# Kernel optimization log

Hardware: AMD Instinct MI355X
Metric: run time of the kernel (lower is better)

Reference implementation:

```python
import jax, jax.numpy as jnp
import numpy as np

N = 100000
E = 3200000
F_IN = 128
H1, C1 = 2, 16          # conv1: heads=2, out_channels=16, concat -> 32
H2, C2 = 1, 40          # conv2: heads=1, out_channels=num_classes=40
NEG_SLOPE = 0.2


def setup_inputs() -> dict:
    key = jax.random.key(0)
    ks = jax.random.split(key, 12)
    features = jax.random.normal(ks[0], (N, F_IN), dtype=jnp.float32)
    edges = jax.random.randint(ks[1], (2, E), 0, N, dtype=jnp.int64)
    weight = jax.random.uniform(ks[2], (E,), dtype=jnp.float32)  # ignored (edge_dim=None)
    s = 0.1
    W1 = jax.random.normal(ks[3], (F_IN, H1 * C1), dtype=jnp.float32) * s
    att_src1 = jax.random.normal(ks[4], (H1, C1), dtype=jnp.float32) * s
    att_dst1 = jax.random.normal(ks[5], (H1, C1), dtype=jnp.float32) * s
    b1 = jnp.zeros((H1 * C1,), dtype=jnp.float32)
    W2 = jax.random.normal(ks[6], (H1 * C1, H2 * C2), dtype=jnp.float32) * s
    att_src2 = jax.random.normal(ks[7], (H2, C2), dtype=jnp.float32) * s
    att_dst2 = jax.random.normal(ks[8], (H2, C2), dtype=jnp.float32) * s
    b2 = jnp.zeros((H2 * C2,), dtype=jnp.float32)
    return {"features": features, "edges": edges, "weight": weight,
            "W1": W1, "att_src1": att_src1, "att_dst1": att_dst1, "b1": b1,
            "W2": W2, "att_src2": att_src2, "att_dst2": att_dst2, "b2": b2}


def _segment_softmax(e, seg, num_segments):
    # e: [E, H]; softmax over edges sharing the same destination node
    m = jax.ops.segment_max(e, seg, num_segments=num_segments)
    ex = jnp.exp(e - m[seg])
    s = jax.ops.segment_sum(ex, seg, num_segments=num_segments)
    return ex / (s[seg] + 1e-16)


def _gat_conv(x, src, dst, W, att_src, att_dst, bias, heads, out_ch):
    n = x.shape[0]
    h = (x @ W).reshape(n, heads, out_ch)                  # [N,H,C]
    a_src = jnp.sum(h * att_src, axis=-1)                  # [N,H]
    a_dst = jnp.sum(h * att_dst, axis=-1)                  # [N,H]
    e = a_src[src] + a_dst[dst]                            # [E,H]
    e = jnp.where(e > 0, e, NEG_SLOPE * e)                 # LeakyReLU(0.2)
    alpha = _segment_softmax(e, dst, n)                    # [E,H]
    msg = h[src] * alpha[:, :, None]                       # [E,H,C]
    out = jax.ops.segment_sum(msg, dst, num_segments=n)    # [N,H,C]
    return out.reshape(n, heads * out_ch) + bias           # concat=True


def reference(features, edges, weight, W1, att_src1, att_dst1, b1,
              W2, att_src2, att_dst2, b2):
    n = features.shape[0]
    # GATConv default add_self_loops=True (self-loop removal of pre-existing
    # loops skipped: negligible for random edges and not jit-shape-friendly)
    loop = jnp.arange(n, dtype=edges.dtype)
    src = jnp.concatenate([edges[0], loop])
    dst = jnp.concatenate([edges[1], loop])
    x = _gat_conv(features, src, dst, W1, att_src1, att_dst1, b1, H1, C1)
    x = jax.nn.relu(x)
    # F.dropout with training=self.training -> identity in eval mode
    x = _gat_conv(x, src, dst, W2, att_src2, att_dst2, b2, H2, C2)
    return x
```

## Files before the change

kernel.cpp:

```cpp
#include <hip/hip_runtime.h>


#define DEVFN __device__ __forceinline__
#define CB_SHIFT 8
#define CB_SZ 256
#define CHUNK 2048
#define HIST_MAX 512
#define A2B 240

DEVFN unsigned short f2h(float f) {
  _Float16 h = (_Float16)f;
  unsigned short u;
  __builtin_memcpy(&u, &h, 2);
  return u;
}
DEVFN float h2f(unsigned short u) {
  _Float16 h;
  __builtin_memcpy(&h, &u, 2);
  return (float)h;
}

DEVFN float lrelu(float e) { return e > 0.f ? e : 0.2f * e; }

DEVFN void acc8(float* acc, float x, uint4 u) {
  acc[0] = fmaf(x, h2f(u.x & 0xffff), acc[0]);
  acc[1] = fmaf(x, h2f(u.x >> 16),    acc[1]);
  acc[2] = fmaf(x, h2f(u.y & 0xffff), acc[2]);
  acc[3] = fmaf(x, h2f(u.y >> 16),    acc[3]);
  acc[4] = fmaf(x, h2f(u.z & 0xffff), acc[4]);
  acc[5] = fmaf(x, h2f(u.z >> 16),    acc[5]);
  acc[6] = fmaf(x, h2f(u.w & 0xffff), acc[6]);
  acc[7] = fmaf(x, h2f(u.w >> 16),    acc[7]);
}

DEVFN void read_edge(const long long* eg64, const int* eg32, int is64, int E,
                     int i, int& s, int& d) {
  if (i >= E) { s = d = i - E; return; }
  if (is64) { s = (int)eg64[i]; d = (int)eg64[E + i]; }
  else      { s = eg32[i];      d = eg32[E + i]; }
}

DEVFN int detect64(const int* eg32, int E, int i0, int t) {
  int base = i0;
  if (base > E - 64) base = E - 64;
  if (base < 0) base = 0;
  int i = base + (t & 63);
  unsigned long long m = __ballot((i < E) && (eg32[2 * i + 1] != 0));
  return m == 0ull;
}

__global__ void scan_blocks(const int* __restrict__ cnt, int* __restrict__ rp,
                            int* __restrict__ bsum, int n) {
  __shared__ int buf[2][1024];
  int t = threadIdx.x;
  int gid = blockIdx.x * 1024 + t;
  int v = (gid < n) ? cnt[gid] : 0;
  buf[0][t] = v;
  __syncthreads();
  int pin = 0;
  for (int offd = 1; offd < 1024; offd <<= 1) {
    int nv = buf[pin][t];
    if (t >= offd) nv += buf[pin][t - offd];
    buf[1 - pin][t] = nv;
    pin = 1 - pin;
    __syncthreads();
  }
  int inc = buf[pin][t];
  if (gid < n) rp[gid] = inc - v;
  if (t == 1023) bsum[blockIdx.x] = inc;
}

__global__ void scan_sums(const int* __restrict__ bsum, int* __restrict__ boff,
                          int nb) {
  __shared__ int buf[2][1024];
  __shared__ int carry;
  int t = threadIdx.x;
  if (t == 0) carry = 0;
  __syncthreads();
  for (int base = 0; base < nb; base += 1024) {
    int v = (base + t < nb) ? bsum[base + t] : 0;
    buf[0][t] = v;
    __syncthreads();
    int pin = 0;
    for (int off = 1; off < 1024; off <<= 1) {
      int nv = buf[pin][t];
      if (t >= off) nv += buf[pin][t - off];
      buf[1 - pin][t] = nv;
      pin = 1 - pin;
      __syncthreads();
    }
    if (base + t < nb) boff[base + t] = carry + buf[pin][t] - v;
    __syncthreads();
    if (t == 0) carry += buf[pin][1023];
    __syncthreads();
  }
}

__global__ void scan_add(int* rp, const int* boff, int n, int total) {
  int i = blockIdx.x * 1024 + threadIdx.x;
  if (i < n) rp[i] = rp[i] + boff[blockIdx.x];
  if (i == 0) rp[n] = total;
}

__global__ __launch_bounds__(256) void chunk_hist(const long long* eg64,
                                                  const int* eg32,
                                                  int E, int N, int NWG,
                                                  int* __restrict__ histg) {
  __shared__ int lh[HIST_MAX];
  int w = blockIdx.x, t = threadIdx.x;
  int NB2 = (N + CB_SZ - 1) / CB_SZ;
  for (int j = t; j < NB2; j += 256) lh[j] = 0;
  int i0 = w * CHUNK;
  int is64 = detect64(eg32, E, i0, t);
  __syncthreads();
  int EN = E + N;
  int i1 = i0 + CHUNK; if (i1 > EN) i1 = EN;
  for (int i = i0 + t; i < i1; i += 256) {
    int d;
    if (i >= E) d = i - E;
    else d = is64 ? (int)eg64[E + i] : eg32[E + i];
    atomicAdd(&lh[d >> CB_SHIFT], 1);
  }
  __syncthreads();
  for (int b = t; b < NB2; b += 256) histg[b * NWG + w] = lh[b];
}

__global__ __launch_bounds__(256) void chunk_scatter(const long long* eg64,
                                                     const int* eg32,
                                                     int E, int N, int NWG,
                                                     const int* __restrict__ hists,
                                                     int* __restrict__ tmp) {
  __shared__ int lcur[HIST_MAX];
  int w = blockIdx.x, t = threadIdx.x;
  int NB2 = (N + CB_SZ - 1) / CB_SZ;
  for (int b = t; b < NB2; b += 256) lcur[b] = hists[b * NWG + w];
  int i0 = w * CHUNK;
  int is64 = detect64(eg32, E, i0, t);
  __syncthreads();
  int EN = E + N;
  int i1 = i0 + CHUNK; if (i1 > EN) i1 = EN;
  for (int i = i0 + t; i < i1; i += 256) {
    int s, d;
    read_edge(eg64, eg32, is64, E, i, s, d);
    int b = d >> CB_SHIFT;
    int pos = atomicAdd(&lcur[b], 1);
    tmp[pos] = (s << CB_SHIFT) | (d & (CB_SZ - 1));
  }
}

__global__ __launch_bounds__(256) void bucket_rp_sort(const int* __restrict__ hists,
                                                      int NWG,
                                                      const int* __restrict__ tmp,
                                                      int* __restrict__ rp,
                                                      int* __restrict__ csr,
                                                      int N, int EN) {
  __shared__ int lc[CB_SZ];
  __shared__ int ps[256];
  __shared__ int lcur[CB_SZ];
  int b = blockIdx.x, t = threadIdx.x;
  lc[t] = 0;
  __syncthreads();
  int w0 = hists[b * NWG];
  int w1 = hists[(b + 1) * NWG];
  for (int p = w0 + t; p < w1; p += 256)
    atomicAdd(&lc[tmp[p] & (CB_SZ - 1)], 1);
  __syncthreads();
  int a = lc[t];
  ps[t] = a;
  __syncthreads();
  for (int off = 1; off < 256; off <<= 1) {
    int v = ps[t];
    int u = (t >= off) ? ps[t - off] : 0;
    __syncthreads();
    ps[t] = v + u;
    __syncthreads();
  }
  int base = w0 + ps[t] - a;
  lcur[t] = base;
  int n0 = b * CB_SZ;
  if (n0 + t < N) rp[n0 + t] = base;
  if (b == (int)gridDim.x - 1 && t == 0) rp[N] = EN;
  __syncthreads();
  for (int p = w0 + t; p < w1; p += 256) {
    int e = tmp[p];
    int pos = atomicAdd(&lcur[e & (CB_SZ - 1)], 1);
    csr[pos] = e >> CB_SHIFT;
  }
}

__global__ __launch_bounds__(256) void gemm1f(const float* __restrict__ X,
                                              const float* __restrict__ W,
                                              const float* __restrict__ att_s,
                                              const float* __restrict__ att_d,
                                              uint4* __restrict__ h1h,
                                              float* __restrict__ as1,
                                              float* __restrict__ ad1, int N) {
  __shared__ float Wl[128 * 32];
  __shared__ float Asl[32], Adl[32];
  int t = threadIdx.x;
  for (int i = t; i < 1024; i += 256)
    ((float4*)Wl)[i] = ((const float4*)W)[i];
  if (t < 32) { Asl[t] = att_s[t]; Adl[t] = att_d[t]; }
  __syncthreads();
  int n = blockIdx.x * 256 + t;
  if (n >= N) return;
  const float4* X4 = (const float4*)(X + (size_t)n * 128);
  float acc[32];
#pragma unroll
  for (int c = 0; c < 32; c++) acc[c] = 0.f;
  for (int k4 = 0; k4 < 32; k4++) {
    float4 x = X4[k4];
    const float4* w4 = (const float4*)(Wl + k4 * 128);
#pragma unroll
    for (int c4 = 0; c4 < 8; c4++) {
      float4 w0 = w4[c4], w1 = w4[8 + c4], w2 = w4[16 + c4], w3 = w4[24 + c4];
      float* A = acc + c4 * 4;
      A[0] = fmaf(x.x, w0.x, A[0]); A[1] = fmaf(x.x, w0.y, A[1]);
      A[2] = fmaf(x.x, w0.z, A[2]); A[3] = fmaf(x.x, w0.w, A[3]);
      A[0] = fmaf(x.y, w1.x, A[0]); A[1] = fmaf(x.y, w1.y, A[1]);
      A[2] = fmaf(x.y, w1.z, A[2]); A[3] = fmaf(x.y, w1.w, A[3]);
      A[0] = fmaf(x.z, w2.x, A[0]); A[1] = fmaf(x.z, w2.y, A[1]);
      A[2] = fmaf(x.z, w2.z, A[2]); A[3] = fmaf(x.z, w2.w, A[3]);
      A[0] = fmaf(x.w, w3.x, A[0]); A[1] = fmaf(x.w, w3.y, A[1]);
      A[2] = fmaf(x.w, w3.z, A[2]); A[3] = fmaf(x.w, w3.w, A[3]);
    }
  }
  float s0 = 0.f, d0 = 0.f, s1 = 0.f, d1 = 0.f;
#pragma unroll
  for (int c = 0; c < 16; c++) {
    s0 = fmaf(acc[c], Asl[c], s0);
    d0 = fmaf(acc[c], Adl[c], d0);
    s1 = fmaf(acc[16 + c], Asl[16 + c], s1);
    d1 = fmaf(acc[16 + c], Adl[16 + c], d1);
  }
  as1[n * 2] = s0; as1[n * 2 + 1] = s1;
  ad1[n * 2] = d0; ad1[n * 2 + 1] = d1;
#pragma unroll
  for (int j = 0; j < 4; j++) {
    uint4 u;
    u.x = (unsigned)f2h(acc[j * 8 + 0]) | ((unsigned)f2h(acc[j * 8 + 1]) << 16);
    u.y = (unsigned)f2h(acc[j * 8 + 2]) | ((unsigned)f2h(acc[j * 8 + 3]) << 16);
    u.z = (unsigned)f2h(acc[j * 8 + 4]) | ((unsigned)f2h(acc[j * 8 + 5]) << 16);
    u.w = (unsigned)f2h(acc[j * 8 + 6]) | ((unsigned)f2h(acc[j * 8 + 7]) << 16);
    h1h[(size_t)n * 4 + j] = u;
  }
}

__global__ __launch_bounds__(256, 8) void agg1_gemm2(
    const int* __restrict__ rp, const int* __restrict__ csr,
    const float* __restrict__ as, const float* __restrict__ ad,
    const uint4* __restrict__ h1h, const float* __restrict__ b1,
    const float* __restrict__ W2, const float* __restrict__ as2w,
    const float* __restrict__ ad2w, uint4* __restrict__ h2h,
    float* __restrict__ as2, float* __restrict__ ad2, int N) {
  __shared__ float Wl[32 * 40];
  __shared__ float As2l[40], Ad2l[40];
  __shared__ float x1t[16][33];
  __shared__ float h2r[16][41];
  int t = threadIdx.x;
  for (int i = t; i < 320; i += 256)
    ((float4*)Wl)[i] = ((const float4*)W2)[i];
  if (t < 40) { As2l[t] = as2w[t]; Ad2l[t] = ad2w[t]; }
  int nl = t >> 4, r = t & 15;
  int half = r >> 2, cq = r & 3;
  int h = cq >> 1;
  int n = blockIdx.x * 16 + nl;
  float acc[8] = {0, 0, 0, 0, 0, 0, 0, 0};
  float ssum = 0.f;
  if (n < N) {
    int p0 = rp[n], p1 = rp[n + 1];
    float adv = ad[n * 2 + h];
    int p = p0 + half;
    for (; p + 12 < p1; p += 16) {
      int sA = csr[p], sB = csr[p + 4], sC = csr[p + 8], sD = csr[p + 12];
      float eA = as[sA * 2 + h] + adv;
      float eB = as[sB * 2 + h] + adv;
      float eC = as[sC * 2 + h] + adv;
      float eD = as[sD * 2 + h] + adv;
      uint4 uA = h1h[(size_t)sA * 4 + cq];
      uint4 uB = h1h[(size_t)sB * 4 + cq];
      uint4 uC = h1h[(size_t)sC * 4 + cq];
      uint4 uD = h1h[(size_t)sD * 4 + cq];
      float xA = __expf(lrelu(eA));
      float xB = __expf(lrelu(eB));
      float xC = __expf(lrelu(eC));
      float xD = __expf(lrelu(eD));
      ssum += (xA + xB) + (xC + xD);
      acc8(acc, xA, uA);
      acc8(acc, xB, uB);
      acc8(acc, xC, uC);
      acc8(acc, xD, uD);
    }
    if (p < p1) {
      bool vB = p + 4 < p1, vC = p + 8 < p1;
      int pB = vB ? p + 4 : p;
      int pC = vC ? p + 8 : p;
      int sA = csr[p], sB = csr[pB], sC = csr[pC];
      float eA = as[sA * 2 + h] + adv;
      float eB = as[sB * 2 + h] + adv;
      float eC = as[sC * 2 + h] + adv;
      uint4 uA = h1h[(size_t)sA * 4 + cq];
      uint4 uB = h1h[(size_t)sB * 4 + cq];
      uint4 uC = h1h[(size_t)sC * 4 + cq];
      float xA = __expf(lrelu(eA));
      float xB = vB ? __expf(lrelu(eB)) : 0.f;
      float xC = vC ? __expf(lrelu(eC)) : 0.f;
      ssum += xA + xB + xC;
      acc8(acc, xA, uA);
      acc8(acc, xB, uB);
      acc8(acc, xC, uC);
    }
  }
#pragma unroll
  for (int j = 0; j < 8; j++) acc[j] += __shfl_xor(acc[j], 4);
  ssum += __shfl_xor(ssum, 4);
#pragma unroll
  for (int j = 0; j < 8; j++) acc[j] += __shfl_xor(acc[j], 8);
  ssum += __shfl_xor(ssum, 8);
  if (n < N && half == 0) {
    float inv = 1.0f / (ssum + 1e-16f);
    float4 ba = ((const float4*)b1)[cq * 2];
    float4 bb = ((const float4*)b1)[cq * 2 + 1];
    int ch0 = cq * 8;
    x1t[nl][ch0 + 0] = fmaxf(fmaf(acc[0], inv, ba.x), 0.f);
    x1t[nl][ch0 + 1] = fmaxf(fmaf(acc[1], inv, ba.y), 0.f);
    x1t[nl][ch0 + 2] = fmaxf(fmaf(acc[2], inv, ba.z), 0.f);
    x1t[nl][ch0 + 3] = fmaxf(fmaf(acc[3], inv, ba.w), 0.f);
    x1t[nl][ch0 + 4] = fmaxf(fmaf(acc[4], inv, bb.x), 0.f);
    x1t[nl][ch0 + 5] = fmaxf(fmaf(acc[5], inv, bb.y), 0.f);
    x1t[nl][ch0 + 6] = fmaxf(fmaf(acc[6], inv, bb.z), 0.f);
    x1t[nl][ch0 + 7] = fmaxf(fmaf(acc[7], inv, bb.w), 0.f);
  }
  __syncthreads();
  if (n < N && r < 8) {
    float acc2[5] = {0, 0, 0, 0, 0};
    int cb = r * 5;
    for (int k = 0; k < 32; k++) {
      float x = x1t[nl][k];
#pragma unroll
      for (int c = 0; c < 5; c++)
        acc2[c] = fmaf(x, Wl[k * 40 + cb + c], acc2[c]);
    }
    float ss = 0.f, sd = 0.f;
#pragma unroll
    for (int c = 0; c < 5; c++) {
      ss = fmaf(acc2[c], As2l[cb + c], ss);
      sd = fmaf(acc2[c], Ad2l[cb + c], sd);
    }
#pragma unroll
    for (int off = 1; off < 8; off <<= 1) {
      ss += __shfl_xor(ss, off);
      sd += __shfl_xor(sd, off);
    }
    if (r == 0) { as2[n] = ss; ad2[n] = sd; }
#pragma unroll
    for (int c = 0; c < 5; c++) h2r[nl][cb + c] = acc2[c];
  }
  __syncthreads();
  if (n < N && r < 5) {
    const float* hr = h2r[nl] + r * 8;
    uint4 u;
    u.x = (unsigned)f2h(hr[0]) | ((unsigned)f2h(hr[1]) << 16);
    u.y = (unsigned)f2h(hr[2]) | ((unsigned)f2h(hr[3]) << 16);
    u.z = (unsigned)f2h(hr[4]) | ((unsigned)f2h(hr[5]) << 16);
    u.w = (unsigned)f2h(hr[6]) | ((unsigned)f2h(hr[7]) << 16);
    h2h[(size_t)n * 8 + r] = u;
  }
}

__global__ __launch_bounds__(256, 8) void agg2_fused(const int* __restrict__ rp,
                                                     const int* __restrict__ csr,
                                                     const float* __restrict__ as,
                                                     const float* __restrict__ ad,
                                                     const uint4* __restrict__ h2h,
                                                     const float* __restrict__ bias,
                                                     float* __restrict__ outp, int N) {
  __shared__ float part[256][9];
  int t = threadIdx.x;
  int idx = blockIdx.x * A2B + t;
  bool act = (t < A2B) && (idx < N * 20);
  int n = 0, half = 0, cq = 0, p0 = 0, p1 = 0;
  float adv = 0.f;
  if (act) {
    n = idx / 20;
    int rr = idx % 20;
    half = rr / 5;
    cq = rr - half * 5;
    p0 = rp[n]; p1 = rp[n + 1];
    adv = ad[n];
  }
  float acc[8] = {0, 0, 0, 0, 0, 0, 0, 0};
  float ssum = 0.f;
  if (act) {
    int p = p0 + half;
    for (; p + 12 < p1; p += 16) {
      int sA = csr[p], sB = csr[p + 4], sC = csr[p + 8], sD = csr[p + 12];
      float eA = as[sA] + adv;
      float eB = as[sB] + adv;
      float eC = as[sC] + adv;
      float eD = as[sD] + adv;
      uint4 uA = h2h[(size_t)sA * 8 + cq];
      uint4 uB = h2h[(size_t)sB * 8 + cq];
      uint4 uC = h2h[(size_t)sC * 8 + cq];
      uint4 uD = h2h[(size_t)sD * 8 + cq];
      float xA = __expf(lrelu(eA));
      float xB = __expf(lrelu(eB));
      float xC = __expf(lrelu(eC));
      float xD = __expf(lrelu(eD));
      ssum += (xA + xB) + (xC + xD);
      acc8(acc, xA, uA);
      acc8(acc, xB, uB);
      acc8(acc, xC, uC);
      acc8(acc, xD, uD);
    }
    if (p < p1) {
      bool vB = p + 4 < p1, vC = p + 8 < p1;
      int pB = vB ? p + 4 : p;
      int pC = vC ? p + 8 : p;
      int sA = csr[p], sB = csr[pB], sC = csr[pC];
      float eA = as[sA] + adv;
      float eB = as[sB] + adv;
      float eC = as[sC] + adv;
      uint4 uA = h2h[(size_t)sA * 8 + cq];
      uint4 uB = h2h[(size_t)sB * 8 + cq];
      uint4 uC = h2h[(size_t)sC * 8 + cq];
      float xA = __expf(lrelu(eA));
      float xB = vB ? __expf(lrelu(eB)) : 0.f;
      float xC = vC ? __expf(lrelu(eC)) : 0.f;
      ssum += xA + xB + xC;
      acc8(acc, xA, uA);
      acc8(acc, xB, uB);
      acc8(acc, xC, uC);
    }
  }
  if (act && half) {
#pragma unroll
    for (int j = 0; j < 8; j++) part[t][j] = acc[j];
    part[t][8] = ssum;
  }
  __syncthreads();
  if (act && half == 0) {
#pragma unroll
    for (int j = 0; j < 8; j++)
      acc[j] += part[t + 5][j] + part[t + 10][j] + part[t + 15][j];
    ssum += part[t + 5][8] + part[t + 10][8] + part[t + 15][8];
    float inv = 1.0f / (ssum + 1e-16f);
    const float4* b4 = (const float4*)bias;
    float4 ba = b4[cq * 2], bb = b4[cq * 2 + 1];
    float4 r0, r1;
    r0.x = fmaf(acc[0], inv, ba.x);
    r0.y = fmaf(acc[1], inv, ba.y);
    r0.z = fmaf(acc[2], inv, ba.z);
    r0.w = fmaf(acc[3], inv, ba.w);
    r1.x = fmaf(acc[4], inv, bb.x);
    r1.y = fmaf(acc[5], inv, bb.y);
    r1.z = fmaf(acc[6], inv, bb.z);
    r1.w = fmaf(acc[7], inv, bb.w);
    ((float4*)outp)[(size_t)n * 10 + cq * 2]     = r0;
    ((float4*)outp)[(size_t)n * 10 + cq * 2 + 1] = r1;
  }
}

extern "C" void kernel_launch(void* const* d_in, const int* in_sizes, int n_in,
                              void* d_out, int out_size, void* d_ws, size_t ws_size,
                              hipStream_t stream) {
  const float* X    = (const float*)d_in[0];
  const long long* eg64 = (const long long*)d_in[1];
  const int* eg32   = (const int*)d_in[1];
  const float* W1   = (const float*)d_in[3];
  const float* as1w = (const float*)d_in[4];
  const float* ad1w = (const float*)d_in[5];
  const float* b1   = (const float*)d_in[6];
  const float* W2   = (const float*)d_in[7];
  const float* as2w = (const float*)d_in[8];
  const float* ad2w = (const float*)d_in[9];
  const float* b2   = (const float*)d_in[10];
  float* out = (float*)d_out;

  const int N  = in_sizes[0] / 128;
  const int E  = in_sizes[1] / 2;
  const int EN = E + N;
  const int NB2 = (N + CB_SZ - 1) / CB_SZ;
  const int NWG = (EN + CHUNK - 1) / CHUNK;
  const int NH  = NB2 * NWG;

  char* wbase = (char*)d_ws;
  size_t off = 0;
  auto alloc = [&](size_t bytes) -> void* {
    void* p = wbase + off;
    off += (bytes + 255) & ~(size_t)255;
    return p;
  };

  uint4* h1h = (uint4*)alloc((size_t)N * 64);
  size_t usz = (size_t)EN * 4;
  if ((size_t)N * 128 > usz) usz = (size_t)N * 128;
  char* uni = (char*)alloc(usz);
  uint4* h2h = (uint4*)uni;
  int*   tmp = (int*)uni;
  float* as1 = (float*)alloc((size_t)N * 2 * 4);
  float* ad1 = (float*)alloc((size_t)N * 2 * 4);
  float* as2 = (float*)alloc((size_t)N * 4);
  float* ad2 = (float*)alloc((size_t)N * 4);
  int* rp     = (int*)alloc((size_t)(N + 1) * 4);
  int* histg  = (int*)alloc((size_t)NH * 4);
  int* hists  = (int*)alloc((size_t)(NH + 1) * 4);
  int* bsum   = (int*)alloc(1024 * 4);
  int* boff   = (int*)alloc(1024 * 4);
  int* csr    = (int*)alloc((size_t)EN * 4);
  (void)ws_size; (void)n_in; (void)out_size;

  const int gN  = (N + 255) / 256;
  const int nbH = (NH + 1023) / 1024;

  chunk_hist<<<NWG, 256, 0, stream>>>(eg64, eg32, E, N, NWG, histg);
  scan_blocks<<<nbH, 1024, 0, stream>>>(histg, hists, bsum, NH);
  scan_sums<<<1, 1024, 0, stream>>>(bsum, boff, nbH);
  scan_add<<<nbH, 1024, 0, stream>>>(hists, boff, NH, EN);
  chunk_scatter<<<NWG, 256, 0, stream>>>(eg64, eg32, E, N, NWG, hists, tmp);
  bucket_rp_sort<<<NB2, 256, 0, stream>>>(hists, NWG, tmp, rp, csr, N, EN);

  gemm1f<<<gN, 256, 0, stream>>>(X, W1, as1w, ad1w, h1h, as1, ad1, N);
  agg1_gemm2<<<(N + 15) / 16, 256, 0, stream>>>(rp, csr, as1, ad1, h1h, b1,
                                                W2, as2w, ad2w, h2h, as2, ad2, N);
  agg2_fused<<<(N * 20 + A2B - 1) / A2B, 256, 0, stream>>>(rp, csr, as2, ad2,
                                                           h2h, b2, out, N);
}
```

Baseline: 358.0 us.

## Replace per-chunk histogram CSR build with global bucket histogram and LDS-sorted scatter

Rebuilds the CSR construction pipeline. A grid-strided global bucket histogram and a single small scan replace the per-chunk histogram matrix and its three-kernel scan. Each scatter block now sorts its 4096-edge chunk by bucket in LDS and claims global slots with one atomic per bucket, so writes to tmp are contiguous. The final per-bucket sort stashes its slice in LDS to avoid re-reading tmp from global memory. The trade-offs are global atomics on bucket cursors, which make the order within a bucket nondeterministic, plus a large LDS footprint that may reduce occupancy.

```diff
diff --git a/kernel.cpp b/kernel.cpp
--- a/kernel.cpp
+++ b/kernel.cpp
@@ -4,8 +4,9 @@
 #define DEVFN __device__ __forceinline__
 #define CB_SHIFT 8
 #define CB_SZ 256
-#define CHUNK 2048
-#define HIST_MAX 512
+#define SC_CHUNK 4096
+#define NBMAX 512
+#define STASH 12288
 #define A2B 240
 
 DEVFN unsigned short f2h(float f) {
@@ -49,107 +50,124 @@
   return m == 0ull;
 }
 
-__global__ void scan_blocks(const int* __restrict__ cnt, int* __restrict__ rp,
-                            int* __restrict__ bsum, int n) {
-  __shared__ int buf[2][1024];
+__global__ __launch_bounds__(256) void bucket_hist(const long long* eg64,
+                                                   const int* eg32,
+                                                   int E, int N, int NB2,
+                                                   int* __restrict__ bhist) {
+  __shared__ int lh[NBMAX];
   int t = threadIdx.x;
-  int gid = blockIdx.x * 1024 + t;
-  int v = (gid < n) ? cnt[gid] : 0;
+  lh[t] = 0; lh[t + 256] = 0;
+  int is64 = detect64(eg32, E, 0, t);
+  __syncthreads();
+  int EN = E + N;
+  int step = (int)gridDim.x * 1024;
+  for (int base = (int)blockIdx.x * 1024; base < EN; base += step) {
+#pragma unroll
+    for (int k = 0; k < 4; k++) {
+      int i = base + k * 256 + t;
+      if (i < EN) {
+        int d;
+        if (i >= E) d = i - E;
+        else d = is64 ? (int)eg64[E + i] : eg32[E + i];
+        atomicAdd(&lh[d >> CB_SHIFT], 1);
+      }
+    }
+  }
+  __syncthreads();
+  if (t < NB2 && lh[t]) atomicAdd(&bhist[t], lh[t]);
+  int t2 = t + 256;
+  if (t2 < NB2 && lh[t2]) atomicAdd(&bhist[t2], lh[t2]);
+}
+
+__global__ void bucket_scan(const int* __restrict__ bhist,
+                            int* __restrict__ bscan, int* __restrict__ gcur,
+                            int NB2, int EN) {
+  __shared__ int buf[2][NBMAX];
+  int t = threadIdx.x;
+  int v = (t < NB2) ? bhist[t] : 0;
   buf[0][t] = v;
   __syncthreads();
   int pin = 0;
-  for (int offd = 1; offd < 1024; offd <<= 1) {
-    int nv = buf[pin][t];
-    if (t >= offd) nv += buf[pin][t - offd];
+  for (int off = 1; off < NBMAX; off <<= 1) {
+    int nv = buf[pin][t] + (t >= off ? buf[pin][t - off] : 0);
     buf[1 - pin][t] = nv;
-    pin = 1 - pin;
+    pin ^= 1;
     __syncthreads();
   }
-  int inc = buf[pin][t];
-  if (gid < n) rp[gid] = inc - v;
-  if (t == 1023) bsum[blockIdx.x] = inc;
-}
-
-__global__ void scan_sums(const int* __restrict__ bsum, int* __restrict__ boff,
-                          int nb) {
-  __shared__ int buf[2][1024];
-  __shared__ int carry;
+  int excl = buf[pin][t] - v;
+  if (t < NB2) { bscan[t] = excl; gcur[t] = excl; }
+  if (t == NB2) bscan[t] = EN;
+}
+
+__global__ __launch_bounds__(256) void chunk_scatter_sorted(
+    const long long* eg64, const int* eg32, int E, int N, int NB2,
+    int* __restrict__ gcur, int* __restrict__ tmp) {
+  __shared__ int lh[NBMAX];
+  __shared__ int lscan[NBMAX];
+  __shared__ int lpos[NBMAX];
+  __shared__ int gbase[NBMAX];
+  __shared__ int sbuf[2][NBMAX];
+  __shared__ int payl[SC_CHUNK];
+  __shared__ unsigned short bktid[SC_CHUNK];
   int t = threadIdx.x;
-  if (t == 0) carry = 0;
-  __syncthreads();
-  for (int base = 0; base < nb; base += 1024) {
-    int v = (base + t < nb) ? bsum[base + t] : 0;
-    buf[0][t] = v;
+  int i0 = (int)blockIdx.x * SC_CHUNK;
+  int is64 = detect64(eg32, E, i0, t);
+  lh[t] = 0; lh[t + 256] = 0;
+  __syncthreads();
+  int EN = E + N;
+  int i1 = i0 + SC_CHUNK; if (i1 > EN) i1 = EN;
+  int total = i1 - i0;
+  int es[16], ed[16];
+#pragma unroll
+  for (int bb = 0; bb < 4; bb++) {
+#pragma unroll
+    for (int k = 0; k < 4; k++) {
+      int idx = bb * 4 + k;
+      int i = i0 + bb * 1024 + k * 256 + t;
+      int s = 0, d = -1;
+      if (i < i1) read_edge(eg64, eg32, is64, E, i, s, d);
+      es[idx] = s; ed[idx] = d;
+    }
+  }
+#pragma unroll
+  for (int j = 0; j < 16; j++)
+    if (ed[j] >= 0) atomicAdd(&lh[ed[j] >> CB_SHIFT], 1);
+  __syncthreads();
+  sbuf[0][t] = lh[t]; sbuf[0][t + 256] = lh[t + 256];
+  __syncthreads();
+  int pin = 0;
+  for (int off = 1; off < NBMAX; off <<= 1) {
+    int nv0 = sbuf[pin][t] + (t >= off ? sbuf[pin][t - off] : 0);
+    int nv1 = sbuf[pin][t + 256] + sbuf[pin][t + 256 - off];
     __syncthreads();
-    int pin = 0;
-    for (int off = 1; off < 1024; off <<= 1) {
-      int nv = buf[pin][t];
-      if (t >= off) nv += buf[pin][t - off];
-      buf[1 - pin][t] = nv;
-      pin = 1 - pin;
-      __syncthreads();
-    }
-    if (base + t < nb) boff[base + t] = carry + buf[pin][t] - v;
+    sbuf[1 - pin][t] = nv0; sbuf[1 - pin][t + 256] = nv1;
+    pin ^= 1;
     __syncthreads();
-    if (t == 0) carry += buf[pin][1023];
-    __syncthreads();
-  }
-}
-
-__global__ void scan_add(int* rp, const int* boff, int n, int total) {
-  int i = blockIdx.x * 1024 + threadIdx.x;
-  if (i < n) rp[i] = rp[i] + boff[blockIdx.x];
-  if (i == 0) rp[n] = total;
-}
-
-__global__ __launch_bounds__(256) void chunk_hist(const long long* eg64,
-                                                  const int* eg32,
-                                                  int E, int N, int NWG,
-                                                  int* __restrict__ histg) {
-  __shared__ int lh[HIST_MAX];
-  int w = blockIdx.x, t = threadIdx.x;
-  int NB2 = (N + CB_SZ - 1) / CB_SZ;
-  for (int j = t; j < NB2; j += 256) lh[j] = 0;
-  int i0 = w * CHUNK;
-  int is64 = detect64(eg32, E, i0, t);
-  __syncthreads();
-  int EN = E + N;
-  int i1 = i0 + CHUNK; if (i1 > EN) i1 = EN;
-  for (int i = i0 + t; i < i1; i += 256) {
-    int d;
-    if (i >= E) d = i - E;
-    else d = is64 ? (int)eg64[E + i] : eg32[E + i];
-    atomicAdd(&lh[d >> CB_SHIFT], 1);
-  }
-  __syncthreads();
-  for (int b = t; b < NB2; b += 256) histg[b * NWG + w] = lh[b];
-}
-
-__global__ __launch_bounds__(256) void chunk_scatter(const long long* eg64,
-                                                     const int* eg32,
-                                                     int E, int N, int NWG,
-                                                     const int* __restrict__ hists,
-                                                     int* __restrict__ tmp) {
-  __shared__ int lcur[HIST_MAX];
-  int w = blockIdx.x, t = threadIdx.x;
-  int NB2 = (N + CB_SZ - 1) / CB_SZ;
-  for (int b = t; b < NB2; b += 256) lcur[b] = hists[b * NWG + w];
-  int i0 = w * CHUNK;
-  int is64 = detect64(eg32, E, i0, t);
-  __syncthreads();
-  int EN = E + N;
-  int i1 = i0 + CHUNK; if (i1 > EN) i1 = EN;
-  for (int i = i0 + t; i < i1; i += 256) {
-    int s, d;
-    read_edge(eg64, eg32, is64, E, i, s, d);
-    int b = d >> CB_SHIFT;
-    int pos = atomicAdd(&lcur[b], 1);
-    tmp[pos] = (s << CB_SHIFT) | (d & (CB_SZ - 1));
-  }
-}
-
-__global__ __launch_bounds__(256) void bucket_rp_sort(const int* __restrict__ hists,
-                                                      int NWG,
+  }
+  lscan[t] = sbuf[pin][t] - lh[t];
+  lscan[t + 256] = sbuf[pin][t + 256] - lh[t + 256];
+  lpos[t] = lscan[t]; lpos[t + 256] = lscan[t + 256];
+  if (t < NB2 && lh[t]) gbase[t] = atomicAdd(&gcur[t], lh[t]);
+  int t2 = t + 256;
+  if (t2 < NB2 && lh[t2]) gbase[t2] = atomicAdd(&gcur[t2], lh[t2]);
+  __syncthreads();
+#pragma unroll
+  for (int j = 0; j < 16; j++) {
+    if (ed[j] >= 0) {
+      int b = ed[j] >> CB_SHIFT;
+      int sl = atomicAdd(&lpos[b], 1);
+      payl[sl] = (es[j] << CB_SHIFT) | (ed[j] & (CB_SZ - 1));
+      bktid[sl] = (unsigned short)b;
+    }
+  }
+  __syncthreads();
+  for (int j = t; j < total; j += 256) {
+    int b = bktid[j];
+    tmp[gbase[b] + (j - lscan[b])] = payl[j];
+  }
+}
+
+__global__ __launch_bounds__(256) void bucket_rp_sort(const int* __restrict__ bscan,
                                                       const int* __restrict__ tmp,
                                                       int* __restrict__ rp,
                                                       int* __restrict__ csr,
@@ -157,13 +175,40 @@
   __shared__ int lc[CB_SZ];
   __shared__ int ps[256];
   __shared__ int lcur[CB_SZ];
+  __shared__ int stash[STASH];
   int b = blockIdx.x, t = threadIdx.x;
   lc[t] = 0;
   __syncthreads();
-  int w0 = hists[b * NWG];
-  int w1 = hists[(b + 1) * NWG];
-  for (int p = w0 + t; p < w1; p += 256)
-    atomicAdd(&lc[tmp[p] & (CB_SZ - 1)], 1);
+  int w0 = bscan[b];
+  int w1 = bscan[b + 1];
+  int cnt = w1 - w0;
+  bool fit = (cnt <= STASH);
+  int p = w0 + t;
+  for (; p + 768 < w1; p += 1024) {
+    int e0 = tmp[p], e1 = tmp[p + 256], e2 = tmp[p + 512], e3 = tmp[p + 768];
+    if (fit) {
+      stash[p - w0] = e0; stash[p - w0 + 256] = e1;
+      stash[p - w0 + 512] = e2; stash[p - w0 + 768] = e3;
+    }
+    atomicAdd(&lc[e0 & (CB_SZ - 1)], 1);
+    atomicAdd(&lc[e1 & (CB_SZ - 1)], 1);
+    atomicAdd(&lc[e2 & (CB_SZ - 1)], 1);
+    atomicAdd(&lc[e3 & (CB_SZ - 1)], 1);
+  }
+  if (p < w1) {
+    bool v1 = p + 256 < w1, v2 = p + 512 < w1;
+    int q1 = v1 ? p + 256 : p;
+    int q2 = v2 ? p + 512 : p;
+    int e0 = tmp[p], e1 = tmp[q1], e2 = tmp[q2];
+    if (fit) {
+      stash[p - w0] = e0;
+      if (v1) stash[q1 - w0] = e1;
+      if (v2) stash[q2 - w0] = e2;
+    }
+    atomicAdd(&lc[e0 & (CB_SZ - 1)], 1);
+    if (v1) atomicAdd(&lc[e1 & (CB_SZ - 1)], 1);
+    if (v2) atomicAdd(&lc[e2 & (CB_SZ - 1)], 1);
+  }
   __syncthreads();
   int a = lc[t];
   ps[t] = a;
@@ -181,10 +226,18 @@
   if (n0 + t < N) rp[n0 + t] = base;
   if (b == (int)gridDim.x - 1 && t == 0) rp[N] = EN;
   __syncthreads();
-  for (int p = w0 + t; p < w1; p += 256) {
-    int e = tmp[p];
-    int pos = atomicAdd(&lcur[e & (CB_SZ - 1)], 1);
-    csr[pos] = e >> CB_SHIFT;
+  if (fit) {
+    for (int j = t; j < cnt; j += 256) {
+      int e = stash[j];
+      int pos = atomicAdd(&lcur[e & (CB_SZ - 1)], 1);
+      csr[pos] = e >> CB_SHIFT;
+    }
+  } else {
+    for (int q = w0 + t; q < w1; q += 256) {
+      int e = tmp[q];
+      int pos = atomicAdd(&lcur[e & (CB_SZ - 1)], 1);
+      csr[pos] = e >> CB_SHIFT;
+    }
   }
 }
 
@@ -481,8 +534,7 @@
   const int E  = in_sizes[1] / 2;
   const int EN = E + N;
   const int NB2 = (N + CB_SZ - 1) / CB_SZ;
-  const int NWG = (EN + CHUNK - 1) / CHUNK;
-  const int NH  = NB2 * NWG;
+  const int NWG = (EN + SC_CHUNK - 1) / SC_CHUNK;
 
   char* wbase = (char*)d_ws;
   size_t off = 0;
@@ -503,22 +555,19 @@
   float* as2 = (float*)alloc((size_t)N * 4);
   float* ad2 = (float*)alloc((size_t)N * 4);
   int* rp     = (int*)alloc((size_t)(N + 1) * 4);
-  int* histg  = (int*)alloc((size_t)NH * 4);
-  int* hists  = (int*)alloc((size_t)(NH + 1) * 4);
-  int* bsum   = (int*)alloc(1024 * 4);
-  int* boff   = (int*)alloc(1024 * 4);
+  int* bhist  = (int*)alloc(NBMAX * 4);
+  int* bscan  = (int*)alloc((NBMAX + 1) * 4);
+  int* gcur   = (int*)alloc(NBMAX * 4);
   int* csr    = (int*)alloc((size_t)EN * 4);
   (void)ws_size; (void)n_in; (void)out_size;
 
-  const int gN  = (N + 255) / 256;
-  const int nbH = (NH + 1023) / 1024;
-
-  chunk_hist<<<NWG, 256, 0, stream>>>(eg64, eg32, E, N, NWG, histg);
-  scan_blocks<<<nbH, 1024, 0, stream>>>(histg, hists, bsum, NH);
-  scan_sums<<<1, 1024, 0, stream>>>(bsum, boff, nbH);
-  scan_add<<<nbH, 1024, 0, stream>>>(hists, boff, NH, EN);
-  chunk_scatter<<<NWG, 256, 0, stream>>>(eg64, eg32, E, N, NWG, hists, tmp);
-  bucket_rp_sort<<<NB2, 256, 0, stream>>>(hists, NWG, tmp, rp, csr, N, EN);
+  const int gN = (N + 255) / 256;
+
+  hipMemsetAsync(bhist, 0, NBMAX * 4, stream);
+  bucket_hist<<<1024, 256, 0, stream>>>(eg64, eg32, E, N, NB2, bhist);
+  bucket_scan<<<1, NBMAX, 0, stream>>>(bhist, bscan, gcur, NB2, EN);
+  chunk_scatter_sorted<<<NWG, 256, 0, stream>>>(eg64, eg32, E, N, NB2, gcur, tmp);
+  bucket_rp_sort<<<NB2, 256, 0, stream>>>(bscan, tmp, rp, csr, N, EN);
 
   gemm1f<<<gN, 256, 0, stream>>>(X, W1, as1w, ad1w, h1h, as1, ad1, N);
   agg1_gemm2<<<(N + 15) / 16, 256, 0, stream>>>(rp, csr, as1, ad1, h1h, b1,
```

Result: faster. 331.7 us (-7.3%).
